# Kernel optimization log

Hardware: AMD Instinct MI355X
Metric: run time of the kernel (lower is better)

The kernel has to match this reference:

```python
import jax, jax.numpy as jnp
import numpy as np

N_NODES, N_EDGES, N_FEAT = 50000, 500000, 128
HID, LAT, N_GRAPHS = 256, 64, 512
HEADS, DH = 8, 32  # GAT: 8 heads x 32 = 256
EPS = 1e-5


def _seg_softmax(logits, seg, num):
    m = jax.ops.segment_max(logits, seg, num_segments=num)
    m = jnp.where(jnp.isfinite(m), m, 0.0)
    e = jnp.exp(logits - m[seg])
    s = jax.ops.segment_sum(e, seg, num_segments=num)
    return e / jnp.maximum(s[seg], 1e-16)


def _bn(h, g, b):  # BatchNorm1d, batch statistics
    mu = h.mean(0)
    var = h.var(0)
    return (h - mu) * jax.lax.rsqrt(var + EPS) * g + b


def _ln(h, g, b):
    mu = h.mean(-1, keepdims=True)
    var = h.var(-1, keepdims=True)
    return (h - mu) * jax.lax.rsqrt(var + EPS) * g + b


def setup_inputs() -> dict:
    key = jax.random.key(0)
    ks = iter(jax.random.split(key, 40))
    f = lambda *s: jax.random.normal(next(ks), s, dtype=jnp.float32) * 0.05
    inp = {
        'x': jax.random.normal(next(ks), (N_NODES, N_FEAT), dtype=jnp.float32),
        'W_emb': f(N_FEAT, HID), 'b_emb': f(HID),
        'W_gcn': f(HID, HID), 'b_gcn': f(HID),
        'W_gat': f(HID, HID), 'a_src': f(HEADS, DH), 'a_dst': f(HEADS, DH), 'b_gat': f(HID),
        'W_l': f(HID, HID), 'b_l': f(HID), 'W_r': f(HID, HID),
        'bn_gamma': jnp.ones((3, HID), jnp.float32), 'bn_beta': jnp.zeros((3, HID), jnp.float32),
        'Wg1': f(HID, HID // 2), 'bg1': f(HID // 2), 'Wg2': f(HID // 2, 1), 'bg2': f(1),
        'Wm1': f(HID, HID), 'bm1': f(HID), 'ln_m_g': jnp.ones(HID, jnp.float32), 'ln_m_b': jnp.zeros(HID, jnp.float32),
        'Wm2': f(HID, LAT), 'bm2': f(LAT),
        'Wv1': f(HID, HID), 'bv1': f(HID), 'ln_v_g': jnp.ones(HID, jnp.float32), 'ln_v_b': jnp.zeros(HID, jnp.float32),
        'Wv2': f(HID, LAT), 'bv2': f(LAT),
        'edge_index': jax.random.randint(next(ks), (2, N_EDGES), 0, N_NODES, dtype=jnp.int64),
        'batch': jnp.sort(jax.random.randint(next(ks), (N_NODES,), 0, N_GRAPHS, dtype=jnp.int64)),
    }
    return inp


def _forward(x, W_emb, b_emb, W_gcn, b_gcn, W_gat, a_src, a_dst, b_gat,
             W_l, b_l, W_r, bn_gamma, bn_beta, Wg1, bg1, Wg2, bg2,
             Wm1, bm1, ln_m_g, ln_m_b, Wm2, bm2, Wv1, bv1, ln_v_g, ln_v_b, Wv2, bv2,
             edge_index, batch):
    N = x.shape[0]
    loops = jnp.arange(N)
    src_sl = jnp.concatenate([edge_index[0], loops])  # with self-loops (GCN/GAT)
    dst_sl = jnp.concatenate([edge_index[1], loops])

    h = x @ W_emb + b_emb  # [N, HID]

    # --- layer 0: GCNConv ---
    deg = jax.ops.segment_sum(jnp.ones_like(dst_sl, dtype=h.dtype), dst_sl, num_segments=N)
    dis = jax.lax.rsqrt(deg)
    norm = dis[src_sl] * dis[dst_sl]  # [E+N]
    xt = h @ W_gcn
    out = jax.ops.segment_sum(xt[src_sl] * norm[:, None], dst_sl, num_segments=N) + b_gcn
    out = jax.nn.relu(_bn(out, bn_gamma[0], bn_beta[0]))
    h = h + out

    # --- layer 1: GATConv (8 heads, concat) ---
    xt = (h @ W_gat).reshape(N, HEADS, DH)
    al_src = (xt * a_src).sum(-1)  # [N, H]
    al_dst = (xt * a_dst).sum(-1)
    logits = jax.nn.leaky_relu(al_src[src_sl] + al_dst[dst_sl], 0.2)  # [E+N, H]
    alpha = _seg_softmax(logits, dst_sl, N)
    out = jax.ops.segment_sum(xt[src_sl] * alpha[:, :, None], dst_sl, num_segments=N)
    out = out.reshape(N, HID) + b_gat
    out = jax.nn.relu(_bn(out, bn_gamma[1], bn_beta[1]))
    h = h + out

    # --- layer 2: SAGEConv (mean aggregation, no self-loops) ---
    src, dst = edge_index[0], edge_index[1]
    cnt = jax.ops.segment_sum(jnp.ones_like(dst, dtype=h.dtype), dst, num_segments=N)
    nb_mean = jax.ops.segment_sum(h[src], dst, num_segments=N) / jnp.maximum(cnt, 1.0)[:, None]
    out = nb_mean @ W_l + b_l + h @ W_r
    out = jax.nn.relu(_bn(out, bn_gamma[2], bn_beta[2]))
    h = h + out

    # --- GlobalAttention pooling ---
    gate = (jax.nn.relu(h @ Wg1 + bg1) @ Wg2 + bg2)[:, 0]  # [N]
    w = _seg_softmax(gate, batch, N_GRAPHS)
    h_graph = jax.ops.segment_sum(h * w[:, None], batch, num_segments=N_GRAPHS)  # [G, HID]

    mu = jax.nn.relu(_ln(h_graph @ Wm1 + bm1, ln_m_g, ln_m_b)) @ Wm2 + bm2
    logvar = jax.nn.relu(_ln(h_graph @ Wv1 + bv1, ln_v_g, ln_v_b)) @ Wv2 + bv2
    return mu, logvar


def reference(x, W_emb, b_emb, W_gcn, b_gcn, W_gat, a_src, a_dst, b_gat,
              W_l, b_l, W_r, bn_gamma, bn_beta, Wg1, bg1, Wg2, bg2,
              Wm1, bm1, ln_m_g, ln_m_b, Wm2, bm2, Wv1, bv1, ln_v_g, ln_v_b, Wv2, bv2,
              edge_index, batch):
    return _forward(x, W_emb, b_emb, W_gcn, b_gcn, W_gat, a_src, a_dst, b_gat,
                    W_l, b_l, W_r, bn_gamma, bn_beta, Wg1, bg1, Wg2, bg2,
                    Wm1, bm1, ln_m_g, ln_m_b, Wm2, bm2, Wv1, bv1, ln_v_g, ln_v_b, Wv2, bv2,
                    edge_index, batch)
```

## Files before the change

kernel.cpp:

```cpp
#include <hip/hip_runtime.h>
#include <cstdint>
#include <cstddef>

#define N_NODES 50000
#define N_EDGES 500000
#define NG 512
#define HID 256
#define EPS 1e-5f
#define SCB 49

typedef __attribute__((ext_vector_type(8))) __bf16 bf16x8;
typedef __attribute__((ext_vector_type(8))) ushort u16x8;
typedef __attribute__((ext_vector_type(4))) float f32x4;

__device__ __forceinline__ ushort f2bf(float f) {
  uint32_t u = __float_as_uint(f);
  uint32_t r = (u + 0x7fffu + ((u >> 16) & 1u)) >> 16;
  return (ushort)r;
}
__device__ __forceinline__ float bfu(ushort u) { return __uint_as_float(((uint32_t)u) << 16); }
__device__ __forceinline__ float4 bf4(ushort4 u) {
  return make_float4(bfu(u.x), bfu(u.y), bfu(u.z), bfu(u.w));
}

__global__ void k_csr_count(const int* __restrict__ ei, int* __restrict__ cnt) {
  int e = blockIdx.x * 256 + threadIdx.x;
  if (e < N_EDGES) atomicAdd(&cnt[ei[N_EDGES + e]], 1);
}

__global__ void k_scan_part(const int* __restrict__ cnt, int* __restrict__ psum) {
  __shared__ int red[256];
  int tid = threadIdx.x;
  int i0 = blockIdx.x * 1024 + tid * 4;
  int s = 0;
  if (i0 + 4 <= N_NODES) {
    int4 v = *reinterpret_cast<const int4*>(cnt + i0);
    s = v.x + v.y + v.z + v.w;
  } else {
    for (int k = 0; k < 4; k++)
      if (i0 + k < N_NODES) s += cnt[i0 + k];
  }
  red[tid] = s;
  __syncthreads();
  for (int o = 128; o > 0; o >>= 1) {
    if (tid < o) red[tid] += red[tid + o];
    __syncthreads();
  }
  if (tid == 0) psum[blockIdx.x] = red[0];
}

__global__ void k_scan_top(const int* __restrict__ psum, int* __restrict__ boff,
                           int* __restrict__ row_ptr) {
  int t = threadIdx.x;
  int v = (t < SCB) ? psum[t] : 0;
  int own = v;
  for (int o = 1; o < 64; o <<= 1) {
    int u = __shfl_up(v, o);
    if (t >= o) v += u;
  }
  if (t < SCB) boff[t] = v - own;
  if (t == 63) row_ptr[N_NODES] = v;
}

__global__ void k_scan_out(const int* __restrict__ cnt, const int* __restrict__ boff,
                           int* __restrict__ row_ptr, float* __restrict__ dis) {
  __shared__ int ps[256];
  int tid = threadIdx.x;
  int i0 = blockIdx.x * 1024 + tid * 4;
  int v[4];
#pragma unroll
  for (int k = 0; k < 4; k++) v[k] = (i0 + k < N_NODES) ? cnt[i0 + k] : 0;
  int s = v[0] + v[1] + v[2] + v[3];
  ps[tid] = s;
  __syncthreads();
  for (int o = 1; o < 256; o <<= 1) {
    int add = (tid >= o) ? ps[tid - o] : 0;
    __syncthreads();
    ps[tid] += add;
    __syncthreads();
  }
  int run = boff[blockIdx.x] + ((tid > 0) ? ps[tid - 1] : 0);
#pragma unroll
  for (int k = 0; k < 4; k++) {
    if (i0 + k < N_NODES) {
      row_ptr[i0 + k] = run;
      dis[i0 + k] = rsqrtf((float)v[k] + 1.0f);
      run += v[k];
    }
  }
}

__global__ void k_csr_fill(const int* __restrict__ ei, const int* __restrict__ row_ptr,
                           int* __restrict__ fill, int* __restrict__ col_src) {
  int e = blockIdx.x * 256 + threadIdx.x;
  if (e >= N_EDGES) return;
  int s = ei[e], d = ei[N_EDGES + e];
  int pos = row_ptr[d] + atomicAdd(&fill[d], 1);
  col_src[pos] = s;
}

struct WtArgs {
  const float* src[6];
  ushort* dst[6];
  int K[6];
  int C[6];
  int off[6];
};

__global__ void k_wt_all(WtArgs a) {
  int b = blockIdx.x;
  int ji = 0;
#pragma unroll
  for (int t = 1; t < 6; t++)
    if (b >= a.off[t]) ji = t;
  int K = a.K[ji], C = a.C[ji];
  int i = (b - a.off[ji]) * 256 + threadIdx.x;
  int c = i / K, k = i - c * K;
  a.dst[ji][i] = f2bf(a.src[ji][k * C + c]);
}

template <int K, int C, bool DUAL, bool AFP32, bool GATE>
__global__ __launch_bounds__(256) void k_mgemm(
    const void* __restrict__ A1v, const ushort* __restrict__ W1t,
    const ushort* __restrict__ A2, const ushort* __restrict__ W2t,
    const float* __restrict__ bias, float* __restrict__ out,
    ushort* __restrict__ out_bf, const float* __restrict__ gw,
    const float* __restrict__ gb, float* __restrict__ gate, int M, int relu) {
  constexpr int KS = K / 32;
  constexpr int CHK = K / 8;
  constexpr int NPAN = C / 64;
  __shared__ ushort wlds[64 * K];
  const int tid = threadIdx.x;
  const int lane = tid & 63;
  const int wid = tid >> 6;
  const int r16 = lane & 15;
  const int kg = lane >> 4;
  const int rbase = blockIdx.x * 64 + wid * 16;

  int arow = rbase + r16;
  if (arow >= M) arow = M - 1;

  bf16x8 af[KS], af2[KS];
  if constexpr (AFP32) {
    const float* ap = (const float*)A1v + (size_t)arow * K + kg * 8;
#pragma unroll
    for (int ks = 0; ks < KS; ks++) {
      float4 lo = *reinterpret_cast<const float4*>(ap + ks * 32);
      float4 hi = *reinterpret_cast<const float4*>(ap + ks * 32 + 4);
      union { u16x8 u; bf16x8 b; } cv;
      cv.u = (u16x8){f2bf(lo.x), f2bf(lo.y), f2bf(lo.z), f2bf(lo.w),
                     f2bf(hi.x), f2bf(hi.y), f2bf(hi.z), f2bf(hi.w)};
      af[ks] = cv.b;
    }
  } else {
    const ushort* ap = (const ushort*)A1v + (size_t)arow * K + kg * 8;
#pragma unroll
    for (int ks = 0; ks < KS; ks++)
      af[ks] = *reinterpret_cast<const bf16x8*>(ap + ks * 32);
  }
  if constexpr (DUAL) {
    const ushort* ap = A2 + (size_t)arow * K + kg * 8;
#pragma unroll
    for (int ks = 0; ks < KS; ks++)
      af2[ks] = *reinterpret_cast<const bf16x8*>(ap + ks * 32);
  }

  float greg[4] = {0.f, 0.f, 0.f, 0.f};

#define STAGE(WT)                                                              \
  {                                                                            \
    _Pragma("unroll") for (int jj = 0; jj < (64 * CHK) / 256; jj++) {          \
      int ci = jj * 256 + tid;                                                 \
      int c = ci / CHK, k16 = ci % CHK;                                        \
      int slot = c * CHK + (k16 ^ (c & 7));                                    \
      *reinterpret_cast<float4*>(&wlds[slot * 8]) =                            \
          *reinterpret_cast<const float4*>(&(WT)[(size_t)(c0 + c) * K + k16 * 8]); \
    }                                                                          \
  }

#define COMPUTE(AF)                                                            \
  {                                                                            \
    _Pragma("unroll") for (int ct = 0; ct < 4; ct++) {                         \
      bf16x8 wf[KS];                                                           \
      int colr = ct * 16 + r16;                                                \
      _Pragma("unroll") for (int ks = 0; ks < KS; ks++) {                      \
        int slot = colr * CHK + ((ks * 4 + kg) ^ (r16 & 7));                   \
        wf[ks] = *reinterpret_cast<const bf16x8*>(&wlds[slot * 8]);            \
      }                                                                        \
      _Pragma("unroll") for (int ks = 0; ks < KS; ks++)                        \
        acc[ct] = __builtin_amdgcn_mfma_f32_16x16x32_bf16((AF)[ks], wf[ks],    \
                                                          acc[ct], 0, 0, 0);   \
    }                                                                          \
  }

#pragma unroll
  for (int pan = 0; pan < NPAN; pan++) {
    const int c0 = pan * 64;
    f32x4 acc[4];
#pragma unroll
    for (int ct = 0; ct < 4; ct++) acc[ct] = (f32x4){0.f, 0.f, 0.f, 0.f};

    if (pan) __syncthreads();
    STAGE(W1t);
    __syncthreads();
    COMPUTE(af);
    if constexpr (DUAL) {
      __syncthreads();
      STAGE(W2t);
      __syncthreads();
      COMPUTE(af2);
    }

    if constexpr (GATE) {
#pragma unroll
      for (int ct = 0; ct < 4; ct++) {
        int col = c0 + ct * 16 + r16;
        float bv = bias[col];
        float wv = gw[col];
#pragma unroll
        for (int i = 0; i < 4; i++) {
          float v = fmaxf(acc[ct][i] + bv, 0.f);
          greg[i] = fmaf(v, wv, greg[i]);
        }
      }
    } else {
#pragma unroll
      for (int ct = 0; ct < 4; ct++) {
        int col = c0 + ct * 16 + r16;
        float bv = bias ? bias[col] : 0.f;
#pragma unroll
        for (int i = 0; i < 4; i++) {
          int row = rbase + kg * 4 + i;
          if (row < M) {
            float v = acc[ct][i] + bv;
            if (relu) v = fmaxf(v, 0.f);
            if (out) out[(size_t)row * C + col] = v;
            if (out_bf) out_bf[(size_t)row * C + col] = f2bf(v);
          }
        }
      }
    }
  }

  if constexpr (GATE) {
#pragma unroll
    for (int i = 0; i < 4; i++) {
#pragma unroll
      for (int o = 1; o < 16; o <<= 1) greg[i] += __shfl_xor(greg[i], o);
    }
    if (r16 == 0) {
      float b0 = gb[0];
#pragma unroll
      for (int i = 0; i < 4; i++) {
        int row = rbase + kg * 4 + i;
        if (row < M) gate[row] = greg[i] + b0;
      }
    }
  }
#undef STAGE
#undef COMPUTE
}

__global__ void k_gcn_agg(const ushort* __restrict__ xt, const float* __restrict__ dis,
                          const int* __restrict__ row_ptr, const int* __restrict__ col_src,
                          const float* __restrict__ b_gcn, ushort* __restrict__ outb) {
  int node = blockIdx.x * 4 + (threadIdx.x >> 6);
  if (node >= N_NODES) return;
  int lane = threadIdx.x & 63;
  int half = lane >> 5;
  int c0 = (lane & 31) * 8;
  float di = dis[node];
  float acc[8];
#pragma unroll
  for (int j = 0; j < 8; j++) acc[j] = 0.f;
  int b = row_ptr[node], e = row_ptr[node + 1];
  int g0 = b;
  for (; g0 + 4 <= e; g0 += 4) {
    int i0 = g0 + half * 2;
    int s0 = col_src[i0], s1 = col_src[i0 + 1];
    float w0 = di * dis[s0], w1 = di * dis[s1];
    u16x8 u0 = *reinterpret_cast<const u16x8*>(xt + (size_t)s0 * HID + c0);
    u16x8 u1 = *reinterpret_cast<const u16x8*>(xt + (size_t)s1 * HID + c0);
#pragma unroll
    for (int j = 0; j < 8; j++) {
      acc[j] = fmaf(bfu(u0[j]), w0, acc[j]);
      acc[j] = fmaf(bfu(u1[j]), w1, acc[j]);
    }
  }
  {
    int i0 = g0 + half * 2;
    int s0 = 0, s1 = 0;
    float w0 = 0.f, w1 = 0.f;
    if (i0 < e) { s0 = col_src[i0]; w0 = di * dis[s0]; }
    if (i0 + 1 < e) { s1 = col_src[i0 + 1]; w1 = di * dis[s1]; }
    u16x8 u0 = *reinterpret_cast<const u16x8*>(xt + (size_t)s0 * HID + c0);
    u16x8 u1 = *reinterpret_cast<const u16x8*>(xt + (size_t)s1 * HID + c0);
#pragma unroll
    for (int j = 0; j < 8; j++) {
      acc[j] = fmaf(bfu(u0[j]), w0, acc[j]);
      acc[j] = fmaf(bfu(u1[j]), w1, acc[j]);
    }
  }
#pragma unroll
  for (int j = 0; j < 8; j++) acc[j] += __shfl_xor(acc[j], 32);
  if (!half) {
    u16x8 un = *reinterpret_cast<const u16x8*>(xt + (size_t)node * HID + c0);
    float w0 = di * di;
    u16x8 r;
#pragma unroll
    for (int j = 0; j < 8; j++) {
      float v = fmaf(bfu(un[j]), w0, acc[j]) + b_gcn[c0 + j];
      r[j] = f2bf(v);
    }
    *reinterpret_cast<u16x8*>(outb + (size_t)node * HID + c0) = r;
  }
}

__global__ void k_gat_al(const ushort* __restrict__ xt, const float* __restrict__ a_src,
                         const float* __restrict__ a_dst, float* __restrict__ alsrc,
                         float* __restrict__ aldst) {
  int node = blockIdx.x * 4 + (threadIdx.x >> 6);
  if (node >= N_NODES) return;
  int lane = threadIdx.x & 63;
  float4 v = bf4(*reinterpret_cast<const ushort4*>(xt + (size_t)node * HID + lane * 4));
  float4 as = *reinterpret_cast<const float4*>(a_src + lane * 4);
  float4 ad = *reinterpret_cast<const float4*>(a_dst + lane * 4);
  float ps = v.x * as.x + v.y * as.y + v.z * as.z + v.w * as.w;
  float pd = v.x * ad.x + v.y * ad.y + v.z * ad.z + v.w * ad.w;
  for (int o = 1; o < 8; o <<= 1) { ps += __shfl_xor(ps, o); pd += __shfl_xor(pd, o); }
  if ((lane & 7) == 0) {
    alsrc[node * 8 + (lane >> 3)] = ps;
    aldst[node * 8 + (lane >> 3)] = pd;
  }
}

__device__ __forceinline__ float leaky02(float x) { return x > 0.f ? x : 0.2f * x; }

__global__ void k_gat_agg(const ushort* __restrict__ xt, const float* __restrict__ alsrc,
                          const float* __restrict__ aldst, const int* __restrict__ row_ptr,
                          const int* __restrict__ col_src, const float* __restrict__ b_gat,
                          ushort* __restrict__ outb) {
  int node = blockIdx.x * 4 + (threadIdx.x >> 6);
  if (node >= N_NODES) return;
  int lane = threadIdx.x & 63;
  int half = lane >> 5;
  int l32 = lane & 31;
  int c0 = l32 * 8;
  int hh = l32 >> 2;
  float ad = aldst[node * 8 + hh];
  float acc[8];
#pragma unroll
  for (int j = 0; j < 8; j++) acc[j] = 0.f;
  float s = 0.f;
  int b = row_ptr[node], e = row_ptr[node + 1];
  int g0 = b;
  for (; g0 + 4 <= e; g0 += 4) {
    int i0 = g0 + half * 2;
    int s0 = col_src[i0], s1 = col_src[i0 + 1];
    float a0 = __expf(leaky02(alsrc[s0 * 8 + hh] + ad));
    float a1 = __expf(leaky02(alsrc[s1 * 8 + hh] + ad));
    u16x8 u0 = *reinterpret_cast<const u16x8*>(xt + (size_t)s0 * HID + c0);
    u16x8 u1 = *reinterpret_cast<const u16x8*>(xt + (size_t)s1 * HID + c0);
    s += a0 + a1;
#pragma unroll
    for (int j = 0; j < 8; j++) {
      acc[j] = fmaf(bfu(u0[j]), a0, acc[j]);
      acc[j] = fmaf(bfu(u1[j]), a1, acc[j]);
    }
  }
  {
    int i0 = g0 + half * 2;
    int s0 = 0, s1 = 0;
    float a0 = 0.f, a1 = 0.f;
    if (i0 < e) { s0 = col_src[i0]; a0 = __expf(leaky02(alsrc[s0 * 8 + hh] + ad)); }
    if (i0 + 1 < e) { s1 = col_src[i0 + 1]; a1 = __expf(leaky02(alsrc[s1 * 8 + hh] + ad)); }
    u16x8 u0 = *reinterpret_cast<const u16x8*>(xt + (size_t)s0 * HID + c0);
    u16x8 u1 = *reinterpret_cast<const u16x8*>(xt + (size_t)s1 * HID + c0);
    s += a0 + a1;
#pragma unroll
    for (int j = 0; j < 8; j++) {
      acc[j] = fmaf(bfu(u0[j]), a0, acc[j]);
      acc[j] = fmaf(bfu(u1[j]), a1, acc[j]);
    }
  }
#pragma unroll
  for (int j = 0; j < 8; j++) acc[j] += __shfl_xor(acc[j], 32);
  s += __shfl_xor(s, 32);
  if (!half) {
    float e0 = __expf(leaky02(alsrc[node * 8 + hh] + ad));
    u16x8 un = *reinterpret_cast<const u16x8*>(xt + (size_t)node * HID + c0);
    float inv_s = 1.0f / (s + e0);
    u16x8 r;
#pragma unroll
    for (int j = 0; j < 8; j++) {
      float v = fmaf(bfu(un[j]), e0, acc[j]) * inv_s + b_gat[c0 + j];
      r[j] = f2bf(v);
    }
    *reinterpret_cast<u16x8*>(outb + (size_t)node * HID + c0) = r;
  }
}

__global__ void k_sage_agg(const ushort* __restrict__ h, const int* __restrict__ row_ptr,
                           const int* __restrict__ col_src, ushort* __restrict__ outb) {
  int node = blockIdx.x * 4 + (threadIdx.x >> 6);
  if (node >= N_NODES) return;
  int lane = threadIdx.x & 63;
  int half = lane >> 5;
  int c0 = (lane & 31) * 8;
  float acc[8];
#pragma unroll
  for (int j = 0; j < 8; j++) acc[j] = 0.f;
  int b = row_ptr[node], e = row_ptr[node + 1];
  int g0 = b;
  for (; g0 + 4 <= e; g0 += 4) {
    int i0 = g0 + half * 2;
    int s0 = col_src[i0], s1 = col_src[i0 + 1];
    u16x8 u0 = *reinterpret_cast<const u16x8*>(h + (size_t)s0 * HID + c0);
    u16x8 u1 = *reinterpret_cast<const u16x8*>(h + (size_t)s1 * HID + c0);
#pragma unroll
    for (int j = 0; j < 8; j++) acc[j] += bfu(u0[j]) + bfu(u1[j]);
  }
  {
    int i0 = g0 + half * 2;
    int s0 = 0, s1 = 0;
    float w0 = 0.f, w1 = 0.f;
    if (i0 < e) { s0 = col_src[i0]; w0 = 1.f; }
    if (i0 + 1 < e) { s1 = col_src[i0 + 1]; w1 = 1.f; }
    u16x8 u0 = *reinterpret_cast<const u16x8*>(h + (size_t)s0 * HID + c0);
    u16x8 u1 = *reinterpret_cast<const u16x8*>(h + (size_t)s1 * HID + c0);
#pragma unroll
    for (int j = 0; j < 8; j++) {
      acc[j] = fmaf(bfu(u0[j]), w0, acc[j]);
      acc[j] = fmaf(bfu(u1[j]), w1, acc[j]);
    }
  }
#pragma unroll
  for (int j = 0; j < 8; j++) acc[j] += __shfl_xor(acc[j], 32);
  if (!half) {
    float inv = 1.0f / fmaxf((float)(e - b), 1.0f);
    u16x8 r;
#pragma unroll
    for (int j = 0; j < 8; j++) r[j] = f2bf(acc[j] * inv);
    *reinterpret_cast<u16x8*>(outb + (size_t)node * HID + c0) = r;
  }
}

__global__ void k_bn_stats(const ushort* __restrict__ x, float* __restrict__ stats) {
  int c = threadIdx.x;
  float s = 0.f, q = 0.f;
  for (int r = blockIdx.x; r < N_NODES; r += gridDim.x) {
    float v = bfu(x[(size_t)r * HID + c]);
    s += v;
    q = fmaf(v, v, q);
  }
  atomicAdd(&stats[c], s);
  atomicAdd(&stats[HID + c], q);
}

__global__ void k_bn_apply(const ushort* __restrict__ x, const float* __restrict__ stats,
                           const float* __restrict__ gamma, const float* __restrict__ beta,
                           float* __restrict__ h, ushort* __restrict__ h_bf) {
  const float invN = 1.0f / (float)N_NODES;
  int total = N_NODES * 64;
  for (int i = blockIdx.x * 256 + threadIdx.x; i < total; i += gridDim.x * 256) {
    int c4 = (i & 63) * 4;
    float4 xv = bf4(*reinterpret_cast<const ushort4*>(x + (size_t)i * 4));
    float4 sm = *reinterpret_cast<const float4*>(stats + c4);
    float4 sq = *reinterpret_cast<const float4*>(stats + HID + c4);
    float4 gm = *reinterpret_cast<const float4*>(gamma + c4);
    float4 bt = *reinterpret_cast<const float4*>(beta + c4);
    float4 hv = *reinterpret_cast<const float4*>(h + (size_t)i * 4);
#define BN1(f)                                                    \
  {                                                               \
    float mu = sm.f * invN;                                       \
    float var = sq.f * invN - mu * mu;                            \
    float sc = gm.f * rsqrtf(var + EPS);                          \
    float v = (xv.f - mu) * sc + bt.f;                            \
    hv.f += fmaxf(v, 0.f);                                        \
  }
    BN1(x) BN1(y) BN1(z) BN1(w)
#undef BN1
    *reinterpret_cast<float4*>(h + (size_t)i * 4) = hv;
    *reinterpret_cast<ushort4*>(h_bf + (size_t)i * 4) =
        make_ushort4(f2bf(hv.x), f2bf(hv.y), f2bf(hv.z), f2bf(hv.w));
  }
}

__global__ void k_gstart(const int* __restrict__ batch, int* __restrict__ gstart) {
  int g = blockIdx.x * 256 + threadIdx.x;
  if (g > NG) return;
  int lo = 0, hi = N_NODES;
  while (lo < hi) {
    int mid = (lo + hi) >> 1;
    if (batch[mid] < g) lo = mid + 1; else hi = mid;
  }
  gstart[g] = lo;
}

__global__ void k_pool(const ushort* __restrict__ hb, const float* __restrict__ gate,
                       const int* __restrict__ gstart, float* __restrict__ hg) {
  __shared__ float red[256];
  __shared__ float wbuf[256];
  int g = blockIdx.x, tid = threadIdx.x;
  int b = gstart[g], e = gstart[g + 1];
  float m = -1e30f;
  for (int r = b + tid; r < e; r += 256) m = fmaxf(m, gate[r]);
  red[tid] = m;
  __syncthreads();
  for (int o = 128; o > 0; o >>= 1) {
    if (tid < o) red[tid] = fmaxf(red[tid], red[tid + o]);
    __syncthreads();
  }
  m = red[0];
  __syncthreads();
  float s = 0.f;
  for (int r = b + tid; r < e; r += 256) s += __expf(gate[r] - m);
  red[tid] = s;
  __syncthreads();
  for (int o = 128; o > 0; o >>= 1) {
    if (tid < o) red[tid] += red[tid + o];
    __syncthreads();
  }
  float inv = 1.0f / fmaxf(red[0], 1e-16f);
  __syncthreads();
  float acc = 0.f;
  for (int cb = b; cb < e; cb += 256) {
    int r = cb + tid;
    wbuf[tid] = (r < e) ? __expf(gate[r] - m) : 0.f;
    __syncthreads();
    int n = min(256, e - cb);
    for (int j = 0; j < n; j++)
      acc = fmaf(bfu(hb[(size_t)(cb + j) * HID + tid]), wbuf[j], acc);
    __syncthreads();
  }
  hg[(size_t)g * HID + tid] = acc * inv;
}

__global__ void k_mlp(const float* __restrict__ hg, const float* __restrict__ W1,
                      const float* __restrict__ b1, const float* __restrict__ lng,
                      const float* __restrict__ lnb, const float* __restrict__ W2,
                      const float* __restrict__ b2, float* __restrict__ out) {
  __shared__ float row[HID];
  __shared__ float z[HID];
  __shared__ float red[HID];
  int g = blockIdx.x, tid = threadIdx.x;
  row[tid] = hg[(size_t)g * HID + tid];
  __syncthreads();
  float acc = b1[tid];
  for (int k = 0; k < HID; k++) acc = fmaf(row[k], W1[(size_t)k * HID + tid], acc);
  red[tid] = acc;
  __syncthreads();
  for (int o = 128; o > 0; o >>= 1) {
    if (tid < o) red[tid] += red[tid + o];
    __syncthreads();
  }
  float mu = red[0] * (1.0f / HID);
  __syncthreads();
  red[tid] = acc * acc;
  __syncthreads();
  for (int o = 128; o > 0; o >>= 1) {
    if (tid < o) red[tid] += red[tid + o];
    __syncthreads();
  }
  float var = red[0] * (1.0f / HID) - mu * mu;
  float zz = (acc - mu) * rsqrtf(var + EPS) * lng[tid] + lnb[tid];
  z[tid] = fmaxf(zz, 0.f);
  __syncthreads();
  if (tid < 64) {
    float o = b2[tid];
    for (int k = 0; k < HID; k++) o = fmaf(z[k], W2[(size_t)k * 64 + tid], o);
    out[(size_t)g * 64 + tid] = o;
  }
}

extern "C" void kernel_launch(void* const* d_in, const int* in_sizes, int n_in,
                              void* d_out, int out_size, void* d_ws, size_t ws_size,
                              hipStream_t stream) {
  const float* x     = (const float*)d_in[0];
  const float* W_emb = (const float*)d_in[1];
  const float* b_emb = (const float*)d_in[2];
  const float* W_gcn = (const float*)d_in[3];
  const float* b_gcn = (const float*)d_in[4];
  const float* W_gat = (const float*)d_in[5];
  const float* a_src = (const float*)d_in[6];
  const float* a_dst = (const float*)d_in[7];
  const float* b_gat = (const float*)d_in[8];
  const float* W_l   = (const float*)d_in[9];
  const float* b_l   = (const float*)d_in[10];
  const float* W_r   = (const float*)d_in[11];
  const float* bn_g  = (const float*)d_in[12];
  const float* bn_b  = (const float*)d_in[13];
  const float* Wg1   = (const float*)d_in[14];
  const float* bg1   = (const float*)d_in[15];
  const float* Wg2   = (const float*)d_in[16];
  const float* bg2   = (const float*)d_in[17];
  const float* Wm1   = (const float*)d_in[18];
  const float* bm1   = (const float*)d_in[19];
  const float* lnmg  = (const float*)d_in[20];
  const float* lnmb  = (const float*)d_in[21];
  const float* Wm2   = (const float*)d_in[22];
  const float* bm2   = (const float*)d_in[23];
  const float* Wv1   = (const float*)d_in[24];
  const float* bv1   = (const float*)d_in[25];
  const float* lnvg  = (const float*)d_in[26];
  const float* lnvb  = (const float*)d_in[27];
  const float* Wv2   = (const float*)d_in[28];
  const float* bv2   = (const float*)d_in[29];
  const int* ei      = (const int*)d_in[30];
  const int* batch   = (const int*)d_in[31];
  float* out = (float*)d_out;

  float* ws = (float*)d_ws;
  float* h     = ws;
  float* t1    = h + (size_t)N_NODES * HID;
  float* alsrc = t1 + (size_t)N_NODES * HID;
  float* aldst = alsrc + N_NODES * 8;
  float* dis   = aldst + N_NODES * 8;
  float* gate  = dis + N_NODES;
  float* hg    = gate + N_NODES;
  float* zbase = hg + NG * HID;
  float* bnst  = zbase;
  int* row_cnt = (int*)(zbase + 3 * 512);
  int* fill    = row_cnt + N_NODES;
  int* row_ptr = fill + N_NODES;
  int* col_src = row_ptr + N_NODES + 1;
  int* gstart  = col_src + N_EDGES;
  int* psum    = gstart + NG + 1;
  int* boff    = psum + 64;

  ushort* t1b = (ushort*)t1;

  size_t off = (size_t)((char*)(boff + 64) - (char*)d_ws);
  off = (off + 15) & ~(size_t)15;
  ushort* h_bf   = (ushort*)((char*)d_ws + off);
  ushort* t0_bf  = h_bf + (size_t)N_NODES * HID;
  ushort* wemb_t = t0_bf + (size_t)N_NODES * HID;
  ushort* wgcn_t = wemb_t + 128 * 256;
  ushort* wgat_t = wgcn_t + 256 * 256;
  ushort* wr_t   = wgat_t + 256 * 256;
  ushort* wl_t   = wr_t + 256 * 256;
  ushort* wg1_t  = wl_t + 256 * 256;

  size_t zbytes = (size_t)3 * 512 * 4 + 2 * (size_t)N_NODES * 4;
  hipMemsetAsync(zbase, 0, zbytes, stream);

  k_csr_count<<<(N_EDGES + 255) / 256, 256, 0, stream>>>(ei, row_cnt);
  k_scan_part<<<SCB, 256, 0, stream>>>(row_cnt, psum);
  k_scan_top<<<1, 64, 0, stream>>>(psum, boff, row_ptr);
  k_scan_out<<<SCB, 256, 0, stream>>>(row_cnt, boff, row_ptr, dis);
  k_csr_fill<<<(N_EDGES + 255) / 256, 256, 0, stream>>>(ei, row_ptr, fill, col_src);

  WtArgs wa;
  wa.src[0] = W_emb; wa.dst[0] = wemb_t; wa.K[0] = 128; wa.C[0] = 256; wa.off[0] = 0;
  wa.src[1] = W_gcn; wa.dst[1] = wgcn_t; wa.K[1] = 256; wa.C[1] = 256; wa.off[1] = 128;
  wa.src[2] = W_gat; wa.dst[2] = wgat_t; wa.K[2] = 256; wa.C[2] = 256; wa.off[2] = 384;
  wa.src[3] = W_r;   wa.dst[3] = wr_t;   wa.K[3] = 256; wa.C[3] = 256; wa.off[3] = 640;
  wa.src[4] = W_l;   wa.dst[4] = wl_t;   wa.K[4] = 256; wa.C[4] = 256; wa.off[4] = 896;
  wa.src[5] = Wg1;   wa.dst[5] = wg1_t;  wa.K[5] = 256; wa.C[5] = 128; wa.off[5] = 1152;
  k_wt_all<<<1280, 256, 0, stream>>>(wa);

  const int RB = (N_NODES + 63) / 64;
  const int AB = (N_NODES + 3) / 4;

  k_mgemm<128, 256, false, true, false><<<RB, 256, 0, stream>>>(
      x, wemb_t, nullptr, nullptr, b_emb, h, h_bf, nullptr, nullptr, nullptr, N_NODES, 0);

  k_mgemm<256, 256, false, false, false><<<RB, 256, 0, stream>>>(
      h_bf, wgcn_t, nullptr, nullptr, nullptr, nullptr, t0_bf, nullptr, nullptr, nullptr, N_NODES, 0);
  k_gcn_agg<<<AB, 256, 0, stream>>>(t0_bf, dis, row_ptr, col_src, b_gcn, t1b);
  k_bn_stats<<<256, 256, 0, stream>>>(t1b, bnst);
  k_bn_apply<<<1024, 256, 0, stream>>>(t1b, bnst, bn_g, bn_b, h, h_bf);

  k_mgemm<256, 256, false, false, false><<<RB, 256, 0, stream>>>(
      h_bf, wgat_t, nullptr, nullptr, nullptr, nullptr, t0_bf, nullptr, nullptr, nullptr, N_NODES, 0);
  k_gat_al<<<AB, 256, 0, stream>>>(t0_bf, a_src, a_dst, alsrc, aldst);
  k_gat_agg<<<AB, 256, 0, stream>>>(t0_bf, alsrc, aldst, row_ptr, col_src, b_gat, t1b);
  k_bn_stats<<<256, 256, 0, stream>>>(t1b, bnst + 512);
  k_bn_apply<<<1024, 256, 0, stream>>>(t1b, bnst + 512, bn_g + HID, bn_b + HID, h, h_bf);

  k_sage_agg<<<AB, 256, 0, stream>>>(h_bf, row_ptr, col_src, t0_bf);
  k_mgemm<256, 256, true, false, false><<<RB, 256, 0, stream>>>(
      h_bf, wr_t, t0_bf, wl_t, b_l, nullptr, t1b, nullptr, nullptr, nullptr, N_NODES, 0);
  k_bn_stats<<<256, 256, 0, stream>>>(t1b, bnst + 1024);
  k_bn_apply<<<1024, 256, 0, stream>>>(t1b, bnst + 1024, bn_g + 2 * HID, bn_b + 2 * HID, h, h_bf);

  k_mgemm<256, 128, false, false, true><<<RB, 256, 0, stream>>>(
      h_bf, wg1_t, nullptr, nullptr, bg1, nullptr, nullptr, Wg2, bg2, gate, N_NODES, 1);
  k_gstart<<<3, 256, 0, stream>>>(batch, gstart);
  k_pool<<<NG, 256, 0, stream>>>(h_bf, gate, gstart, hg);

  k_mlp<<<NG, 256, 0, stream>>>(hg, Wm1, bm1, lnmg, lnmb, Wm2, bm2, out);
  k_mlp<<<NG, 256, 0, stream>>>(hg, Wv1, bv1, lnvg, lnvb, Wv2, bv2, out + (size_t)NG * 64);
}
```

Before: 654.3 us.

## Drop fp32 residual copy and prefetch next weight panel in GEMM

The fp32 residual array h is removed. bn_apply now reads the residual from the bf16 copy and writes only bf16, and the embedding GEMM no longer writes fp32 output, which cuts global traffic on every layer. The GEMM also loads the next 64-column weight panel into registers while the current panel computes, then writes it to LDS after a barrier, so global load latency overlaps MFMA work. The residual stream now accumulates in bf16, which lowers precision across the three layers, and the prefetch raises register pressure.

New measurement: 715.4 us. +9.3%, slower.

```diff
diff --git a/kernel.cpp b/kernel.cpp
--- a/kernel.cpp
+++ b/kernel.cpp
@@ -123,12 +123,14 @@
 __global__ __launch_bounds__(256) void k_mgemm(
     const void* __restrict__ A1v, const ushort* __restrict__ W1t,
     const ushort* __restrict__ A2, const ushort* __restrict__ W2t,
-    const float* __restrict__ bias, float* __restrict__ out,
-    ushort* __restrict__ out_bf, const float* __restrict__ gw,
-    const float* __restrict__ gb, float* __restrict__ gate, int M, int relu) {
+    const float* __restrict__ bias, ushort* __restrict__ out_bf,
+    const float* __restrict__ gw, const float* __restrict__ gb,
+    float* __restrict__ gate, int M, int relu) {
   constexpr int KS = K / 32;
   constexpr int CHK = K / 8;
   constexpr int NPAN = C / 64;
+  constexpr int NLD = (64 * CHK) / 256;
+  constexpr int NTOT = NPAN * (DUAL ? 2 : 1);
   __shared__ ushort wlds[64 * K];
   const int tid = threadIdx.x;
   const int lane = tid & 63;
@@ -165,18 +167,17 @@
       af2[ks] = *reinterpret_cast<const bf16x8*>(ap + ks * 32);
   }
 
+  int srcoff[NLD], slotv[NLD];
+#pragma unroll
+  for (int jj = 0; jj < NLD; jj++) {
+    int cc = (jj * 256 + tid) / CHK;
+    int k16 = (jj * 256 + tid) % CHK;
+    srcoff[jj] = cc * K + k16 * 8;
+    slotv[jj] = (cc * CHK + (k16 ^ (cc & 7))) * 8;
+  }
+
   float greg[4] = {0.f, 0.f, 0.f, 0.f};
-
-#define STAGE(WT)                                                              \
-  {                                                                            \
-    _Pragma("unroll") for (int jj = 0; jj < (64 * CHK) / 256; jj++) {          \
-      int ci = jj * 256 + tid;                                                 \
-      int c = ci / CHK, k16 = ci % CHK;                                        \
-      int slot = c * CHK + (k16 ^ (c & 7));                                    \
-      *reinterpret_cast<float4*>(&wlds[slot * 8]) =                            \
-          *reinterpret_cast<const float4*>(&(WT)[(size_t)(c0 + c) * K + k16 * 8]); \
-    }                                                                          \
-  }
+  f32x4 acc[4];
 
 #define COMPUTE(AF)                                                            \
   {                                                                            \
@@ -193,52 +194,76 @@
     }                                                                          \
   }
 
-#pragma unroll
-  for (int pan = 0; pan < NPAN; pan++) {
+  {
+    float4 preg[NLD];
+#pragma unroll
+    for (int jj = 0; jj < NLD; jj++)
+      preg[jj] = *reinterpret_cast<const float4*>(W1t + srcoff[jj]);
+#pragma unroll
+    for (int jj = 0; jj < NLD; jj++)
+      *reinterpret_cast<float4*>(&wlds[slotv[jj]]) = preg[jj];
+  }
+  __syncthreads();
+
+#pragma unroll
+  for (int q = 0; q < NTOT; q++) {
+    const int pan = DUAL ? (q >> 1) : q;
+    const int pass = DUAL ? (q & 1) : 0;
     const int c0 = pan * 64;
-    f32x4 acc[4];
-#pragma unroll
-    for (int ct = 0; ct < 4; ct++) acc[ct] = (f32x4){0.f, 0.f, 0.f, 0.f};
-
-    if (pan) __syncthreads();
-    STAGE(W1t);
-    __syncthreads();
-    COMPUTE(af);
-    if constexpr (DUAL) {
-      __syncthreads();
-      STAGE(W2t);
-      __syncthreads();
+    if (pass == 0) {
+#pragma unroll
+      for (int ct = 0; ct < 4; ct++) acc[ct] = (f32x4){0.f, 0.f, 0.f, 0.f};
+    }
+    float4 nreg[NLD];
+    if (q + 1 < NTOT) {
+      const int npan = DUAL ? ((q + 1) >> 1) : (q + 1);
+      const ushort* Wq = (DUAL && ((q + 1) & 1)) ? W2t : W1t;
+      const ushort* base = Wq + (size_t)(npan * 64) * K;
+#pragma unroll
+      for (int jj = 0; jj < NLD; jj++)
+        nreg[jj] = *reinterpret_cast<const float4*>(base + srcoff[jj]);
+    }
+    if (DUAL && pass) {
       COMPUTE(af2);
-    }
-
-    if constexpr (GATE) {
-#pragma unroll
-      for (int ct = 0; ct < 4; ct++) {
-        int col = c0 + ct * 16 + r16;
-        float bv = bias[col];
-        float wv = gw[col];
-#pragma unroll
-        for (int i = 0; i < 4; i++) {
-          float v = fmaxf(acc[ct][i] + bv, 0.f);
-          greg[i] = fmaf(v, wv, greg[i]);
+    } else {
+      COMPUTE(af);
+    }
+    if (pass == (DUAL ? 1 : 0)) {
+      if constexpr (GATE) {
+#pragma unroll
+        for (int ct = 0; ct < 4; ct++) {
+          int col = c0 + ct * 16 + r16;
+          float bv = bias[col];
+          float wv = gw[col];
+#pragma unroll
+          for (int i = 0; i < 4; i++) {
+            float v = fmaxf(acc[ct][i] + bv, 0.f);
+            greg[i] = fmaf(v, wv, greg[i]);
+          }
         }
-      }
-    } else {
-#pragma unroll
-      for (int ct = 0; ct < 4; ct++) {
-        int col = c0 + ct * 16 + r16;
-        float bv = bias ? bias[col] : 0.f;
-#pragma unroll
-        for (int i = 0; i < 4; i++) {
-          int row = rbase + kg * 4 + i;
-          if (row < M) {
-            float v = acc[ct][i] + bv;
-            if (relu) v = fmaxf(v, 0.f);
-            if (out) out[(size_t)row * C + col] = v;
-            if (out_bf) out_bf[(size_t)row * C + col] = f2bf(v);
+      } else {
+#pragma unroll
+        for (int ct = 0; ct < 4; ct++) {
+          int col = c0 + ct * 16 + r16;
+          float bv = bias ? bias[col] : 0.f;
+#pragma unroll
+          for (int i = 0; i < 4; i++) {
+            int row = rbase + kg * 4 + i;
+            if (row < M) {
+              float v = acc[ct][i] + bv;
+              if (relu) v = fmaxf(v, 0.f);
+              out_bf[(size_t)row * C + col] = f2bf(v);
+            }
           }
         }
       }
+    }
+    __syncthreads();
+    if (q + 1 < NTOT) {
+#pragma unroll
+      for (int jj = 0; jj < NLD; jj++)
+        *reinterpret_cast<float4*>(&wlds[slotv[jj]]) = nreg[jj];
+      __syncthreads();
     }
   }
 
@@ -257,7 +282,6 @@
       }
     }
   }
-#undef STAGE
 #undef COMPUTE
 }
 
@@ -459,7 +483,7 @@
 
 __global__ void k_bn_apply(const ushort* __restrict__ x, const float* __restrict__ stats,
                            const float* __restrict__ gamma, const float* __restrict__ beta,
-                           float* __restrict__ h, ushort* __restrict__ h_bf) {
+                           ushort* __restrict__ h_bf) {
   const float invN = 1.0f / (float)N_NODES;
   int total = N_NODES * 64;
   for (int i = blockIdx.x * 256 + threadIdx.x; i < total; i += gridDim.x * 256) {
@@ -469,7 +493,7 @@
     float4 sq = *reinterpret_cast<const float4*>(stats + HID + c4);
     float4 gm = *reinterpret_cast<const float4*>(gamma + c4);
     float4 bt = *reinterpret_cast<const float4*>(beta + c4);
-    float4 hv = *reinterpret_cast<const float4*>(h + (size_t)i * 4);
+    float4 hv = bf4(*reinterpret_cast<const ushort4*>(h_bf + (size_t)i * 4));
 #define BN1(f)                                                    \
   {                                                               \
     float mu = sm.f * invN;                                       \
@@ -480,7 +504,6 @@
   }
     BN1(x) BN1(y) BN1(z) BN1(w)
 #undef BN1
-    *reinterpret_cast<float4*>(h + (size_t)i * 4) = hv;
     *reinterpret_cast<ushort4*>(h_bf + (size_t)i * 4) =
         make_ushort4(f2bf(hv.x), f2bf(hv.y), f2bf(hv.z), f2bf(hv.w));
   }
@@ -663,29 +686,29 @@
   const int AB = (N_NODES + 3) / 4;
 
   k_mgemm<128, 256, false, true, false><<<RB, 256, 0, stream>>>(
-      x, wemb_t, nullptr, nullptr, b_emb, h, h_bf, nullptr, nullptr, nullptr, N_NODES, 0);
+      x, wemb_t, nullptr, nullptr, b_emb, h_bf, nullptr, nullptr, nullptr, N_NODES, 0);
 
   k_mgemm<256, 256, false, false, false><<<RB, 256, 0, stream>>>(
-      h_bf, wgcn_t, nullptr, nullptr, nullptr, nullptr, t0_bf, nullptr, nullptr, nullptr, N_NODES, 0);
+      h_bf, wgcn_t, nullptr, nullptr, nullptr, t0_bf, nullptr, nullptr, nullptr, N_NODES, 0);
   k_gcn_agg<<<AB, 256, 0, stream>>>(t0_bf, dis, row_ptr, col_src, b_gcn, t1b);
   k_bn_stats<<<256, 256, 0, stream>>>(t1b, bnst);
-  k_bn_apply<<<1024, 256, 0, stream>>>(t1b, bnst, bn_g, bn_b, h, h_bf);
+  k_bn_apply<<<1024, 256, 0, stream>>>(t1b, bnst, bn_g, bn_b, h_bf);
 
   k_mgemm<256, 256, false, false, false><<<RB, 256, 0, stream>>>(
-      h_bf, wgat_t, nullptr, nullptr, nullptr, nullptr, t0_bf, nullptr, nullptr, nullptr, N_NODES, 0);
+      h_bf, wgat_t, nullptr, nullptr, nullptr, t0_bf, nullptr, nullptr, nullptr, N_NODES, 0);
   k_gat_al<<<AB, 256, 0, stream>>>(t0_bf, a_src, a_dst, alsrc, aldst);
   k_gat_agg<<<AB, 256, 0, stream>>>(t0_bf, alsrc, aldst, row_ptr, col_src, b_gat, t1b);
   k_bn_stats<<<256, 256, 0, stream>>>(t1b, bnst + 512);
-  k_bn_apply<<<1024, 256, 0, stream>>>(t1b, bnst + 512, bn_g + HID, bn_b + HID, h, h_bf);
+  k_bn_apply<<<1024, 256, 0, stream>>>(t1b, bnst + 512, bn_g + HID, bn_b + HID, h_bf);
 
   k_sage_agg<<<AB, 256, 0, stream>>>(h_bf, row_ptr, col_src, t0_bf);
   k_mgemm<256, 256, true, false, false><<<RB, 256, 0, stream>>>(
-      h_bf, wr_t, t0_bf, wl_t, b_l, nullptr, t1b, nullptr, nullptr, nullptr, N_NODES, 0);
+      h_bf, wr_t, t0_bf, wl_t, b_l, t1b, nullptr, nullptr, nullptr, N_NODES, 0);
   k_bn_stats<<<256, 256, 0, stream>>>(t1b, bnst + 1024);
-  k_bn_apply<<<1024, 256, 0, stream>>>(t1b, bnst + 1024, bn_g + 2 * HID, bn_b + 2 * HID, h, h_bf);
+  k_bn_apply<<<1024, 256, 0, stream>>>(t1b, bnst + 1024, bn_g + 2 * HID, bn_b + 2 * HID, h_bf);
 
   k_mgemm<256, 128, false, false, true><<<RB, 256, 0, stream>>>(
-      h_bf, wg1_t, nullptr, nullptr, bg1, nullptr, nullptr, Wg2, bg2, gate, N_NODES, 1);
+      h_bf, wg1_t, nullptr, nullptr, bg1, nullptr, Wg2, bg2, gate, N_NODES, 1);
   k_gstart<<<3, 256, 0, stream>>>(batch, gstart);
   k_pool<<<NG, 256, 0, stream>>>(h_bf, gate, gstart, hg);
 
```
